# Performance work log

Measured on AMD Instinct MI355X. Metric: run time of the kernel, lower is better.

## Reference

```python
import jax, jax.numpy as jnp
import numpy as np

TEMPERATURE = 8.0  # sqrt(d_k=64)

def setup_inputs() -> dict:
    key = jax.random.key(0)
    kq, kk, kv, km1, km2 = jax.random.split(key, 5)
    B, Lq, Lk, D = 128, 512, 512, 64
    q = jax.random.normal(kq, (B, Lq, D), dtype=jnp.float32)
    k = jax.random.normal(kk, (B, Lk, D), dtype=jnp.float32)
    v = jax.random.normal(kv, (B, Lk, D), dtype=jnp.float32)
    key_mask = jax.random.bernoulli(km1, 0.5, (B, Lq, Lk))
    query_mask = jax.random.bernoulli(km2, 0.5, (B, Lq, Lk))
    return {"q": q, "k": k, "v": v, "key_mask": key_mask, "query_mask": query_mask}

def reference(q, k, v, key_mask, query_mask):
    # attn = (q @ k^T) / temperature, pre-softmax key masking with -inf
    scores = jnp.einsum('bqd,bkd->bqk', q, k) / TEMPERATURE
    scores = jnp.where(key_mask, -jnp.inf, scores)
    attn = jax.nn.softmax(scores, axis=-1)
    # post-softmax query-row zeroing
    attn = jnp.where(query_mask, 0.0, attn)
    # dropout omitted (eval mode / deterministic reference)
    output = jnp.einsum('bqk,bkd->bqd', attn, v)
    return (output, attn)
```

## Files before the change

### kernel.cpp

```cpp
#include <hip/hip_runtime.h>
#include <hip/hip_bf16.h>

#define BATCH 128
#define LQ    512
#define LK    512
#define DH    64
#define TQ    16
#define SSTR  520
#define VROW  72

#define WS_K 0
#define WS_V 4194304
#define WS_Q 8388608
#define WS_BYTES 25165824ull

typedef float    float4v __attribute__((ext_vector_type(4)));
typedef short    short8v __attribute__((ext_vector_type(8)));
typedef short    short4v __attribute__((ext_vector_type(4)));
typedef int      int4v   __attribute__((ext_vector_type(4)));
typedef _Float16 half4v  __attribute__((ext_vector_type(4)));

__device__ __forceinline__ short bf16r(float f) {
  union { float f; unsigned u; } x; x.f = f;
  unsigned r = x.u + 0x7FFFu + ((x.u >> 16) & 1u);
  return (short)(r >> 16);
}

__global__ __launch_bounds__(256)
void prep_kernel(const float* __restrict__ Q, const float* __restrict__ K,
                 const float* __restrict__ V, short* __restrict__ ws)
{
  const int bid = blockIdx.x, tid = threadIdx.x;
  if (bid < 1024) {
    __shared__ short T[64 * VROW];
    const int b  = bid >> 3;
    const int k0 = (bid & 7) * 64;
    const int bR = tid >> 4;
    const int bC = tid & 15;
    const float* vp = V + ((size_t)(b * LK + k0 + bR * 4)) * DH + bC * 4;
    float4v r0 = *(const float4v*)(vp);
    float4v r1 = *(const float4v*)(vp + DH);
    float4v r2 = *(const float4v*)(vp + 2 * DH);
    float4v r3 = *(const float4v*)(vp + 3 * DH);
#pragma unroll
    for (int e = 0; e < 4; ++e) {
      int d  = bC * 4 + e;
      int gp = bR ^ (d & 15);
      short4v s4;
      s4[0] = bf16r(r0[e]); s4[1] = bf16r(r1[e]);
      s4[2] = bf16r(r2[e]); s4[3] = bf16r(r3[e]);
      *(short4v*)&T[d * VROW + gp * 4] = s4;
    }
    __syncthreads();
    const int d  = tid >> 2;
    const int g0 = (tid & 3) * 4;
    short v16[16];
#pragma unroll
    for (int s2 = 0; s2 < 4; ++s2) {
      int g = g0 + s2;
      short4v t4 = *(const short4v*)&T[d * VROW + ((g ^ (d & 15)) * 4)];
      v16[s2 * 4 + 0] = t4[0]; v16[s2 * 4 + 1] = t4[1];
      v16[s2 * 4 + 2] = t4[2]; v16[s2 * 4 + 3] = t4[3];
    }
    short* dst = ws + WS_V + ((size_t)(b * DH + d)) * LK + k0 + g0 * 4;
    *(short8v*)(dst)     = *(short8v*)&v16[0];
    *(short8v*)(dst + 8) = *(short8v*)&v16[8];
  } else {
    const bool isK = (bid < 1152);
    const size_t base = (size_t)((isK ? bid - 1024 : bid - 1152)) * 32768;
    const float* src = (isK ? K : Q) + base;
    short* dst = ws + (isK ? WS_K : WS_Q) + base;
#pragma unroll 4
    for (int u = 0; u < 32; ++u) {
      float4v f = *(const float4v*)(src + u * 1024 + tid * 4);
      short4v s4;
      s4[0] = bf16r(f[0]); s4[1] = bf16r(f[1]);
      s4[2] = bf16r(f[2]); s4[3] = bf16r(f[3]);
      *(short4v*)(dst + u * 1024 + tid * 4) = s4;
    }
  }
}

__global__ __launch_bounds__(256, 4)
void sdpa_main(const short* __restrict__ Kbf, const short* __restrict__ Vt,
               const short* __restrict__ Qbf, const int* __restrict__ KM,
               const int* __restrict__ QM, float* __restrict__ OUT,
               float* __restrict__ ATT)
{
  __shared__ short sc[TQ * SSTR];
  __shared__ float cmb[2][64];

  const int bid  = blockIdx.x;
  const int wg   = ((bid & 7) << 9) | (bid >> 3);
  const int b    = wg >> 5;
  const int q0   = (wg & 31) * TQ;
  const int tid  = threadIdx.x;
  const int lane = tid & 63;
  const int wv   = tid >> 6;
  const int lm   = lane & 15;
  const int quad = lane >> 4;

  const size_t qg    = (size_t)(b * LQ + q0 + lm);
  const size_t mbase = qg * LK + wv * 128 + quad * 4;

  int4v kmv[8];
#pragma unroll
  for (int t = 0; t < 8; ++t)
    kmv[t] = __builtin_nontemporal_load((const int4v*)(KM + mbase + t * 16));

  const short* qp = Qbf + qg * DH + quad * 8;
  const short8v qb0 = *(const short8v*)(qp);
  const short8v qb1 = *(const short8v*)(qp + 32);

  float s[32];
  const short* kp0 = Kbf + ((size_t)(b * LK + wv * 128 + lm)) * DH + quad * 8;
#pragma unroll
  for (int t = 0; t < 8; ++t) {
    const short* kp = kp0 + (size_t)t * 16 * DH;
    short8v ka0 = *(const short8v*)(kp);
    short8v ka1 = *(const short8v*)(kp + 32);
    float4v acc = {0.f, 0.f, 0.f, 0.f};
    acc = __builtin_amdgcn_mfma_f32_16x16x32_bf16(ka0, qb0, acc, 0, 0, 0);
    acc = __builtin_amdgcn_mfma_f32_16x16x32_bf16(ka1, qb1, acc, 0, 0, 0);
#pragma unroll
    for (int j = 0; j < 4; ++j) s[t * 4 + j] = acc[j];
  }

  float mx0 = -INFINITY, mx1 = -INFINITY, mx2 = -INFINITY, mx3 = -INFINITY;
#pragma unroll
  for (int t = 0; t < 8; ++t) {
#pragma unroll
    for (int e = 0; e < 4; ++e) {
      float v = kmv[t][e] ? -INFINITY : s[t * 4 + e];
      s[t * 4 + e] = v;
      if (e == 0) mx0 = fmaxf(mx0, v);
      else if (e == 1) mx1 = fmaxf(mx1, v);
      else if (e == 2) mx2 = fmaxf(mx2, v);
      else mx3 = fmaxf(mx3, v);
    }
  }
  float mx = fmaxf(fmaxf(mx0, mx1), fmaxf(mx2, mx3));
  mx = fmaxf(mx, __shfl_xor(mx, 16, 64));
  mx = fmaxf(mx, __shfl_xor(mx, 32, 64));

  int4v qmv[8];
#pragma unroll
  for (int t = 0; t < 8; ++t)
    qmv[t] = __builtin_nontemporal_load((const int4v*)(QM + mbase + t * 16));

  if (lane < 16) cmb[0][wv * 16 + lane] = mx;
  __syncthreads();
  mx = fmaxf(fmaxf(cmb[0][lm], cmb[0][16 + lm]),
             fmaxf(cmb[0][32 + lm], cmb[0][48 + lm]));

  float s0 = 0.f, s1 = 0.f, s2 = 0.f, s3 = 0.f;
#pragma unroll
  for (int t = 0; t < 8; ++t) {
    float p0 = __expf((s[t * 4 + 0] - mx) * 0.125f);
    float p1 = __expf((s[t * 4 + 1] - mx) * 0.125f);
    float p2 = __expf((s[t * 4 + 2] - mx) * 0.125f);
    float p3 = __expf((s[t * 4 + 3] - mx) * 0.125f);
    s[t * 4 + 0] = p0; s[t * 4 + 1] = p1;
    s[t * 4 + 2] = p2; s[t * 4 + 3] = p3;
    s0 += p0; s1 += p1; s2 += p2; s3 += p3;
  }
  float sum = (s0 + s1) + (s2 + s3);
  sum += __shfl_xor(sum, 16, 64);
  sum += __shfl_xor(sum, 32, 64);
  if (lane < 16) cmb[1][wv * 16 + lane] = sum;
  __syncthreads();
  sum = (cmb[1][lm] + cmb[1][16 + lm]) + (cmb[1][32 + lm] + cmb[1][48 + lm]);
  const float inv = __builtin_amdgcn_rcpf(sum);

  float* arow = ATT + mbase;
  short* srow = &sc[lm * SSTR + wv * 128 + quad * 4];
#pragma unroll
  for (int t = 0; t < 8; ++t) {
    float4v a4;
#pragma unroll
    for (int e = 0; e < 4; ++e)
      a4[e] = qmv[t][e] ? 0.f : s[t * 4 + e] * inv;
    __builtin_nontemporal_store(a4, (float4v*)(arow + t * 16));
    short4v ab;
    ab[0] = bf16r(a4[0]); ab[1] = bf16r(a4[1]);
    ab[2] = bf16r(a4[2]); ab[3] = bf16r(a4[3]);
    *(short4v*)(srow + t * 16) = ab;
  }
  __syncthreads();

  float4v oa = {0.f, 0.f, 0.f, 0.f}, ob = {0.f, 0.f, 0.f, 0.f};
  const short* ap = &sc[lm * SSTR + quad * 8];
  const short* vp = Vt + ((size_t)(b * DH + wv * 16 + lm)) * LK + quad * 8;
#pragma unroll
  for (int c = 0; c < 16; c += 2) {
    short8v a0 = *(const short8v*)(ap + c * 32);
    short8v b0 = *(const short8v*)(vp + c * 32);
    short8v a1 = *(const short8v*)(ap + (c + 1) * 32);
    short8v b1 = *(const short8v*)(vp + (c + 1) * 32);
    oa = __builtin_amdgcn_mfma_f32_16x16x32_bf16(a0, b0, oa, 0, 0, 0);
    ob = __builtin_amdgcn_mfma_f32_16x16x32_bf16(a1, b1, ob, 0, 0, 0);
  }
  float4v oacc = oa + ob;
  float* obase = OUT + ((size_t)(b * LQ + q0 + quad * 4)) * DH + wv * 16 + lm;
  obase[0 * DH] = oacc[0];
  obase[1 * DH] = oacc[1];
  obase[2 * DH] = oacc[2];
  obase[3 * DH] = oacc[3];
}

__global__ __launch_bounds__(256, 4)
void sdpa_fallback(const float* __restrict__ Q, const float* __restrict__ K,
                   const float* __restrict__ V, const int* __restrict__ KM,
                   const int* __restrict__ QM, float* __restrict__ OUT,
                   float* __restrict__ ATT)
{
  __shared__ short kvs[64 * VROW];
  __shared__ short scs[TQ * SSTR];
  const int bid  = blockIdx.x;
  const int wg   = ((bid & 7) << 9) | (bid >> 3);
  const int b    = wg >> 5;
  const int q0   = (wg & 31) * TQ;
  const int tid  = threadIdx.x;
  const int lane = tid & 63;
  const int wave = tid >> 6;
  const int lm   = lane & 15;
  const int quad = lane >> 4;
  const int row  = tid >> 4;
  const int col  = tid & 15;
  const size_t gro = (size_t)(b * LQ + q0 + row) * LK;
  int4v km8[8];
#pragma unroll
  for (int j = 0; j < 8; ++j)
    km8[j] = __builtin_nontemporal_load((const int4v*)(KM + gro + col * 4 + j * 64));
  const float* qrow = Q + ((size_t)(b * LQ + q0 + lm)) * DH + quad * 8;
  short8v aq0, aq1;
  {
    float4v f0 = *(const float4v*)(qrow + 0);
    float4v f1 = *(const float4v*)(qrow + 4);
    float4v f2 = *(const float4v*)(qrow + 32);
    float4v f3 = *(const float4v*)(qrow + 36);
#pragma unroll
    for (int e = 0; e < 4; ++e) {
      aq0[e] = bf16r(f0[e]); aq0[e + 4] = bf16r(f1[e]);
      aq1[e] = bf16r(f2[e]); aq1[e + 4] = bf16r(f3[e]);
    }
  }
  unsigned kb = 0;
#pragma unroll
  for (int j = 0; j < 8; ++j)
#pragma unroll
    for (int e = 0; e < 4; ++e) kb |= (unsigned)(km8[j][e] != 0) << (j * 4 + e);
  const float* kbp = K + ((size_t)(b * LK + lm)) * DH + quad * 8;
#pragma unroll
  for (int t = 0; t < 8; ++t) {
    const float* kr = kbp + (size_t)(wave * 8 + t) * 16 * DH;
    float4v f0 = *(const float4v*)(kr + 0);
    float4v f1 = *(const float4v*)(kr + 4);
    float4v f2 = *(const float4v*)(kr + 32);
    float4v f3 = *(const float4v*)(kr + 36);
    short8v b0, b1;
#pragma unroll
    for (int e = 0; e < 4; ++e) {
      b0[e] = bf16r(f0[e]); b0[e + 4] = bf16r(f1[e]);
      b1[e] = bf16r(f2[e]); b1[e + 4] = bf16r(f3[e]);
    }
    float4v acc = {0.f, 0.f, 0.f, 0.f};
    acc = __builtin_amdgcn_mfma_f32_16x16x32_bf16(aq0, b0, acc, 0, 0, 0);
    acc = __builtin_amdgcn_mfma_f32_16x16x32_bf16(aq1, b1, acc, 0, 0, 0);
    const int n = (wave * 8 + t) * 16 + lm;
#pragma unroll
    for (int j = 0; j < 4; ++j)
      *(_Float16*)&scs[(quad * 4 + j) * SSTR + n] = (_Float16)acc[j];
  }
  int4v qm8[8];
#pragma unroll
  for (int j = 0; j < 8; ++j)
    qm8[j] = __builtin_nontemporal_load((const int4v*)(QM + gro + col * 4 + j * 64));
  __syncthreads();
  float s[32];
  float mx = -INFINITY;
#pragma unroll
  for (int j = 0; j < 8; ++j) {
    half4v h4 = *(const half4v*)&scs[row * SSTR + col * 4 + j * 64];
#pragma unroll
    for (int e = 0; e < 4; ++e) {
      float val = ((kb >> (j * 4 + e)) & 1u) ? -INFINITY : (float)h4[e];
      s[j * 4 + e] = val;
      mx = fmaxf(mx, val);
    }
  }
#pragma unroll
  for (int off = 8; off; off >>= 1) mx = fmaxf(mx, __shfl_xor(mx, off, 64));
  unsigned qb = 0;
#pragma unroll
  for (int j = 0; j < 8; ++j)
#pragma unroll
    for (int e = 0; e < 4; ++e) qb |= (unsigned)(qm8[j][e] != 0) << (j * 4 + e);
  float sum = 0.f;
#pragma unroll
  for (int j = 0; j < 32; ++j) {
    float p = __expf((s[j] - mx) * 0.125f);
    s[j] = p; sum += p;
  }
#pragma unroll
  for (int off = 8; off; off >>= 1) sum += __shfl_xor(sum, off, 64);
  const float inv = 1.f / sum;
  float* arow = ATT + gro;
#pragma unroll
  for (int j = 0; j < 8; ++j) {
    int kk = col * 4 + j * 64;
    float4v a4;
#pragma unroll
    for (int e = 0; e < 4; ++e)
      a4[e] = ((qb >> (j * 4 + e)) & 1u) ? 0.f : s[j * 4 + e] * inv;
    *(float4v*)(arow + kk) = a4;
    short4v ab;
    ab[0] = bf16r(a4[0]); ab[1] = bf16r(a4[1]);
    ab[2] = bf16r(a4[2]); ab[3] = bf16r(a4[3]);
    *(short4v*)&scs[row * SSTR + kk] = ab;
  }
  float4v oacc = {0.f, 0.f, 0.f, 0.f};
  const float* vbase = V + ((size_t)b * LK) * DH;
#pragma unroll
  for (int kt = 0; kt < 8; ++kt) {
    const float* vp = vbase + (kt * 64 + row * 4) * DH + col * 4;
    float4v r0 = *(const float4v*)(vp);
    float4v r1 = *(const float4v*)(vp + DH);
    float4v r2 = *(const float4v*)(vp + 2 * DH);
    float4v r3 = *(const float4v*)(vp + 3 * DH);
#pragma unroll
    for (int e = 0; e < 4; ++e) {
      int d = col * 4 + e;
      int gp = row ^ (d & 15);
      short4v s4;
      s4[0] = bf16r(r0[e]); s4[1] = bf16r(r1[e]);
      s4[2] = bf16r(r2[e]); s4[3] = bf16r(r3[e]);
      *(short4v*)&kvs[d * VROW + gp * 4] = s4;
    }
    __syncthreads();
#pragma unroll
    for (int ks = 0; ks < 2; ++ks) {
      const short* ap = &scs[lm * SSTR + kt * 64 + ks * 32 + quad * 8];
      short8v a8 = *(const short8v*)ap;
      int n  = wave * 16 + lm;
      int g0 = ks * 8 + quad * 2;
      short4v lo = *(const short4v*)&kvs[n * VROW + ((g0) ^ (n & 15)) * 4];
      short4v hi = *(const short4v*)&kvs[n * VROW + ((g0 + 1) ^ (n & 15)) * 4];
      short8v b8;
      b8[0] = lo[0]; b8[1] = lo[1]; b8[2] = lo[2]; b8[3] = lo[3];
      b8[4] = hi[0]; b8[5] = hi[1]; b8[6] = hi[2]; b8[7] = hi[3];
      oacc = __builtin_amdgcn_mfma_f32_16x16x32_bf16(a8, b8, oacc, 0, 0, 0);
    }
    __syncthreads();
  }
  float* obase = OUT + ((size_t)(b * LQ + q0 + quad * 4)) * DH + wave * 16 + lm;
  obase[0 * DH] = oacc[0];
  obase[1 * DH] = oacc[1];
  obase[2 * DH] = oacc[2];
  obase[3 * DH] = oacc[3];
}

extern "C" void kernel_launch(void* const* d_in, const int* in_sizes, int n_in,
                              void* d_out, int out_size, void* d_ws, size_t ws_size,
                              hipStream_t stream) {
  const float* q  = (const float*)d_in[0];
  const float* k  = (const float*)d_in[1];
  const float* v  = (const float*)d_in[2];
  const int*   km = (const int*)d_in[3];
  const int*   qm = (const int*)d_in[4];
  float* out  = (float*)d_out;
  float* attn = out + (size_t)BATCH * LQ * DH;
  if (d_ws != nullptr && ws_size >= WS_BYTES) {
    short* ws = (short*)d_ws;
    hipLaunchKernelGGL(prep_kernel, dim3(1280), dim3(256), 0, stream, q, k, v, ws);
    hipLaunchKernelGGL(sdpa_main, dim3(BATCH * (LQ / TQ)), dim3(256), 0, stream,
                       ws + WS_K, ws + WS_V, ws + WS_Q, km, qm, out, attn);
  } else {
    hipLaunchKernelGGL(sdpa_fallback, dim3(BATCH * (LQ / TQ)), dim3(256), 0, stream,
                       q, k, v, km, qm, out, attn);
  }
}
```

Measured before the change: 422.4 us.

## Pack boolean masks into bitfields in prep kernel before main attention pass

Adds mask-packing blocks to the prep kernel that read both int32 masks and write them as 32-bit bitfields into the workspace. The main kernel then loads one word per lane per mask instead of eight 16-byte vectors each. The aim is to cut register pressure and load latency in the main kernel. In exchange the full mask bytes are still read once, plus an extra write and read of the packed masks. Attention stores also switch from nontemporal to regular, and a raw-mask variant is kept for smaller workspaces.

```diff
diff --git a/kernel.cpp b/kernel.cpp
--- a/kernel.cpp
+++ b/kernel.cpp
@@ -12,7 +12,9 @@
 #define WS_K 0
 #define WS_V 4194304
 #define WS_Q 8388608
-#define WS_BYTES 25165824ull
+#define WS_MB_SHORT 12582912
+#define WS_BYTES_QKV 25165824ull
+#define WS_BYTES_FULL 33554432ull
 
 typedef float    float4v __attribute__((ext_vector_type(4)));
 typedef short    short8v __attribute__((ext_vector_type(8)));
@@ -28,7 +30,8 @@
 
 __global__ __launch_bounds__(256)
 void prep_kernel(const float* __restrict__ Q, const float* __restrict__ K,
-                 const float* __restrict__ V, short* __restrict__ ws)
+                 const float* __restrict__ V, const int* __restrict__ KM,
+                 const int* __restrict__ QM, short* __restrict__ ws)
 {
   const int bid = blockIdx.x, tid = threadIdx.x;
   if (bid < 1024) {
@@ -65,7 +68,7 @@
     short* dst = ws + WS_V + ((size_t)(b * DH + d)) * LK + k0 + g0 * 4;
     *(short8v*)(dst)     = *(short8v*)&v16[0];
     *(short8v*)(dst + 8) = *(short8v*)&v16[8];
-  } else {
+  } else if (bid < 1280) {
     const bool isK = (bid < 1152);
     const size_t base = (size_t)((isK ? bid - 1024 : bid - 1152)) * 32768;
     const float* src = (isK ? K : Q) + base;
@@ -78,14 +81,38 @@
       s4[2] = bf16r(f[2]); s4[3] = bf16r(f[3]);
       *(short4v*)(dst + u * 1024 + tid * 4) = s4;
     }
+  } else {
+    const bool isKM = (bid < 2304);
+    const int  mi   = bid - (isKM ? 1280 : 2304);
+    const int  b    = mi >> 3;
+    const int  q0   = (mi & 7) * 64;
+    const int  ql   = tid >> 2;
+    const int  wv   = tid & 3;
+    const int* src  = (isKM ? KM : QM) +
+                      ((size_t)(b * LQ + q0 + ql)) * LK + wv * 128;
+    unsigned bits[4] = {0u, 0u, 0u, 0u};
+#pragma unroll
+    for (int t = 0; t < 8; ++t) {
+#pragma unroll
+      for (int quad = 0; quad < 4; ++quad) {
+        int4v m4 = *(const int4v*)(src + t * 16 + quad * 4);
+#pragma unroll
+        for (int e = 0; e < 4; ++e)
+          bits[quad] |= (unsigned)(m4[e] != 0) << (t * 4 + e);
+      }
+    }
+    unsigned* mb = (unsigned*)(ws + WS_MB_SHORT) + (isKM ? 0u : 1048576u);
+    *(int4v*)(mb + ((size_t)(b * LQ + q0 + ql)) * 16 + wv * 4) =
+        *(const int4v*)bits;
   }
 }
 
 __global__ __launch_bounds__(256, 4)
-void sdpa_main(const short* __restrict__ Kbf, const short* __restrict__ Vt,
-               const short* __restrict__ Qbf, const int* __restrict__ KM,
-               const int* __restrict__ QM, float* __restrict__ OUT,
-               float* __restrict__ ATT)
+void sdpa_main_packed(const short* __restrict__ Kbf, const short* __restrict__ Vt,
+                      const short* __restrict__ Qbf,
+                      const unsigned* __restrict__ KMB,
+                      const unsigned* __restrict__ QMB,
+                      float* __restrict__ OUT, float* __restrict__ ATT)
 {
   __shared__ short sc[TQ * SSTR];
   __shared__ float cmb[2][64];
@@ -103,10 +130,8 @@
   const size_t qg    = (size_t)(b * LQ + q0 + lm);
   const size_t mbase = qg * LK + wv * 128 + quad * 4;
 
-  int4v kmv[8];
-#pragma unroll
-  for (int t = 0; t < 8; ++t)
-    kmv[t] = __builtin_nontemporal_load((const int4v*)(KM + mbase + t * 16));
+  const unsigned kb  = KMB[qg * 16 + wv * 4 + quad];
+  const unsigned qmb = QMB[qg * 16 + wv * 4 + quad];
 
   const short* qp = Qbf + qg * DH + quad * 8;
   const short8v qb0 = *(const short8v*)(qp);
@@ -131,7 +156,7 @@
   for (int t = 0; t < 8; ++t) {
 #pragma unroll
     for (int e = 0; e < 4; ++e) {
-      float v = kmv[t][e] ? -INFINITY : s[t * 4 + e];
+      float v = ((kb >> (t * 4 + e)) & 1u) ? -INFINITY : s[t * 4 + e];
       s[t * 4 + e] = v;
       if (e == 0) mx0 = fmaxf(mx0, v);
       else if (e == 1) mx1 = fmaxf(mx1, v);
@@ -142,12 +167,6 @@
   float mx = fmaxf(fmaxf(mx0, mx1), fmaxf(mx2, mx3));
   mx = fmaxf(mx, __shfl_xor(mx, 16, 64));
   mx = fmaxf(mx, __shfl_xor(mx, 32, 64));
-
-  int4v qmv[8];
-#pragma unroll
-  for (int t = 0; t < 8; ++t)
-    qmv[t] = __builtin_nontemporal_load((const int4v*)(QM + mbase + t * 16));
-
   if (lane < 16) cmb[0][wv * 16 + lane] = mx;
   __syncthreads();
   mx = fmaxf(fmaxf(cmb[0][lm], cmb[0][16 + lm]),
@@ -179,8 +198,8 @@
     float4v a4;
 #pragma unroll
     for (int e = 0; e < 4; ++e)
-      a4[e] = qmv[t][e] ? 0.f : s[t * 4 + e] * inv;
-    __builtin_nontemporal_store(a4, (float4v*)(arow + t * 16));
+      a4[e] = ((qmb >> (t * 4 + e)) & 1u) ? 0.f : s[t * 4 + e] * inv;
+    *(float4v*)(arow + t * 16) = a4;
     short4v ab;
     ab[0] = bf16r(a4[0]); ab[1] = bf16r(a4[1]);
     ab[2] = bf16r(a4[2]); ab[3] = bf16r(a4[3]);
@@ -188,6 +207,113 @@
   }
   __syncthreads();
 
+  float4v oa = {0.f, 0.f, 0.f, 0.f}, ob = {0.f, 0.f, 0.f, 0.f};
+  const short* ap = &sc[lm * SSTR + quad * 8];
+  const short* vp = Vt + ((size_t)(b * DH + wv * 16 + lm)) * LK + quad * 8;
+#pragma unroll
+  for (int c = 0; c < 16; c += 2) {
+    short8v a0 = *(const short8v*)(ap + c * 32);
+    short8v b0 = *(const short8v*)(vp + c * 32);
+    short8v a1 = *(const short8v*)(ap + (c + 1) * 32);
+    short8v b1 = *(const short8v*)(vp + (c + 1) * 32);
+    oa = __builtin_amdgcn_mfma_f32_16x16x32_bf16(a0, b0, oa, 0, 0, 0);
+    ob = __builtin_amdgcn_mfma_f32_16x16x32_bf16(a1, b1, ob, 0, 0, 0);
+  }
+  float4v oacc = oa + ob;
+  float* obase = OUT + ((size_t)(b * LQ + q0 + quad * 4)) * DH + wv * 16 + lm;
+  obase[0 * DH] = oacc[0];
+  obase[1 * DH] = oacc[1];
+  obase[2 * DH] = oacc[2];
+  obase[3 * DH] = oacc[3];
+}
+
+__global__ __launch_bounds__(256, 4)
+void sdpa_main_raw(const short* __restrict__ Kbf, const short* __restrict__ Vt,
+                   const short* __restrict__ Qbf, const int* __restrict__ KM,
+                   const int* __restrict__ QM, float* __restrict__ OUT,
+                   float* __restrict__ ATT)
+{
+  __shared__ short sc[TQ * SSTR];
+  __shared__ float cmb[2][64];
+  const int bid  = blockIdx.x;
+  const int wg   = ((bid & 7) << 9) | (bid >> 3);
+  const int b    = wg >> 5;
+  const int q0   = (wg & 31) * TQ;
+  const int tid  = threadIdx.x;
+  const int lane = tid & 63;
+  const int wv   = tid >> 6;
+  const int lm   = lane & 15;
+  const int quad = lane >> 4;
+  const size_t qg    = (size_t)(b * LQ + q0 + lm);
+  const size_t mbase = qg * LK + wv * 128 + quad * 4;
+  int4v kmv[8];
+#pragma unroll
+  for (int t = 0; t < 8; ++t)
+    kmv[t] = __builtin_nontemporal_load((const int4v*)(KM + mbase + t * 16));
+  const short* qp = Qbf + qg * DH + quad * 8;
+  const short8v qb0 = *(const short8v*)(qp);
+  const short8v qb1 = *(const short8v*)(qp + 32);
+  float s[32];
+  const short* kp0 = Kbf + ((size_t)(b * LK + wv * 128 + lm)) * DH + quad * 8;
+#pragma unroll
+  for (int t = 0; t < 8; ++t) {
+    const short* kp = kp0 + (size_t)t * 16 * DH;
+    short8v ka0 = *(const short8v*)(kp);
+    short8v ka1 = *(const short8v*)(kp + 32);
+    float4v acc = {0.f, 0.f, 0.f, 0.f};
+    acc = __builtin_amdgcn_mfma_f32_16x16x32_bf16(ka0, qb0, acc, 0, 0, 0);
+    acc = __builtin_amdgcn_mfma_f32_16x16x32_bf16(ka1, qb1, acc, 0, 0, 0);
+#pragma unroll
+    for (int j = 0; j < 4; ++j) s[t * 4 + j] = acc[j];
+  }
+  float mx = -INFINITY;
+#pragma unroll
+  for (int t = 0; t < 8; ++t)
+#pragma unroll
+    for (int e = 0; e < 4; ++e) {
+      float v = kmv[t][e] ? -INFINITY : s[t * 4 + e];
+      s[t * 4 + e] = v;
+      mx = fmaxf(mx, v);
+    }
+  mx = fmaxf(mx, __shfl_xor(mx, 16, 64));
+  mx = fmaxf(mx, __shfl_xor(mx, 32, 64));
+  int4v qmv[8];
+#pragma unroll
+  for (int t = 0; t < 8; ++t)
+    qmv[t] = __builtin_nontemporal_load((const int4v*)(QM + mbase + t * 16));
+  if (lane < 16) cmb[0][wv * 16 + lane] = mx;
+  __syncthreads();
+  mx = fmaxf(fmaxf(cmb[0][lm], cmb[0][16 + lm]),
+             fmaxf(cmb[0][32 + lm], cmb[0][48 + lm]));
+  float sum = 0.f;
+#pragma unroll
+  for (int t = 0; t < 8; ++t)
+#pragma unroll
+    for (int e = 0; e < 4; ++e) {
+      float p = __expf((s[t * 4 + e] - mx) * 0.125f);
+      s[t * 4 + e] = p; sum += p;
+    }
+  sum += __shfl_xor(sum, 16, 64);
+  sum += __shfl_xor(sum, 32, 64);
+  if (lane < 16) cmb[1][wv * 16 + lane] = sum;
+  __syncthreads();
+  sum = (cmb[1][lm] + cmb[1][16 + lm]) + (cmb[1][32 + lm] + cmb[1][48 + lm]);
+  const float inv = __builtin_amdgcn_rcpf(sum);
+  float* arow = ATT + mbase;
+  short* srow = &sc[lm * SSTR + wv * 128 + quad * 4];
+#pragma unroll
+  for (int t = 0; t < 8; ++t) {
+    float4v a4;
+#pragma unroll
+    for (int e = 0; e < 4; ++e)
+      a4[e] = qmv[t][e] ? 0.f : s[t * 4 + e] * inv;
+    *(float4v*)(arow + t * 16) = a4;
+    short4v ab;
+    ab[0] = bf16r(a4[0]); ab[1] = bf16r(a4[1]);
+    ab[2] = bf16r(a4[2]); ab[3] = bf16r(a4[3]);
+    *(short4v*)(srow + t * 16) = ab;
+  }
+  __syncthreads();
   float4v oa = {0.f, 0.f, 0.f, 0.f}, ob = {0.f, 0.f, 0.f, 0.f};
   const short* ap = &sc[lm * SSTR + quad * 8];
   const short* vp = Vt + ((size_t)(b * DH + wv * 16 + lm)) * LK + quad * 8;
@@ -231,7 +357,7 @@
   int4v km8[8];
 #pragma unroll
   for (int j = 0; j < 8; ++j)
-    km8[j] = __builtin_nontemporal_load((const int4v*)(KM + gro + col * 4 + j * 64));
+    km8[j] = *(const int4v*)(KM + gro + col * 4 + j * 64);
   const float* qrow = Q + ((size_t)(b * LQ + q0 + lm)) * DH + quad * 8;
   short8v aq0, aq1;
   {
@@ -245,11 +371,11 @@
       aq1[e] = bf16r(f2[e]); aq1[e + 4] = bf16r(f3[e]);
     }
   }
-  unsigned kb = 0;
+  unsigned kbm = 0;
 #pragma unroll
   for (int j = 0; j < 8; ++j)
 #pragma unroll
-    for (int e = 0; e < 4; ++e) kb |= (unsigned)(km8[j][e] != 0) << (j * 4 + e);
+    for (int e = 0; e < 4; ++e) kbm |= (unsigned)(km8[j][e] != 0) << (j * 4 + e);
   const float* kbp = K + ((size_t)(b * LK + lm)) * DH + quad * 8;
 #pragma unroll
   for (int t = 0; t < 8; ++t) {
@@ -275,7 +401,7 @@
   int4v qm8[8];
 #pragma unroll
   for (int j = 0; j < 8; ++j)
-    qm8[j] = __builtin_nontemporal_load((const int4v*)(QM + gro + col * 4 + j * 64));
+    qm8[j] = *(const int4v*)(QM + gro + col * 4 + j * 64);
   __syncthreads();
   float s[32];
   float mx = -INFINITY;
@@ -284,18 +410,18 @@
     half4v h4 = *(const half4v*)&scs[row * SSTR + col * 4 + j * 64];
 #pragma unroll
     for (int e = 0; e < 4; ++e) {
-      float val = ((kb >> (j * 4 + e)) & 1u) ? -INFINITY : (float)h4[e];
+      float val = ((kbm >> (j * 4 + e)) & 1u) ? -INFINITY : (float)h4[e];
       s[j * 4 + e] = val;
       mx = fmaxf(mx, val);
     }
   }
 #pragma unroll
   for (int off = 8; off; off >>= 1) mx = fmaxf(mx, __shfl_xor(mx, off, 64));
-  unsigned qb = 0;
+  unsigned qbm = 0;
 #pragma unroll
   for (int j = 0; j < 8; ++j)
 #pragma unroll
-    for (int e = 0; e < 4; ++e) qb |= (unsigned)(qm8[j][e] != 0) << (j * 4 + e);
+    for (int e = 0; e < 4; ++e) qbm |= (unsigned)(qm8[j][e] != 0) << (j * 4 + e);
   float sum = 0.f;
 #pragma unroll
   for (int j = 0; j < 32; ++j) {
@@ -312,7 +438,7 @@
     float4v a4;
 #pragma unroll
     for (int e = 0; e < 4; ++e)
-      a4[e] = ((qb >> (j * 4 + e)) & 1u) ? 0.f : s[j * 4 + e] * inv;
+      a4[e] = ((qbm >> (j * 4 + e)) & 1u) ? 0.f : s[j * 4 + e] * inv;
     *(float4v*)(arow + kk) = a4;
     short4v ab;
     ab[0] = bf16r(a4[0]); ab[1] = bf16r(a4[1]);
@@ -370,13 +496,24 @@
   const int*   qm = (const int*)d_in[4];
   float* out  = (float*)d_out;
   float* attn = out + (size_t)BATCH * LQ * DH;
-  if (d_ws != nullptr && ws_size >= WS_BYTES) {
+  if (d_ws != nullptr && ws_size >= WS_BYTES_FULL) {
     short* ws = (short*)d_ws;
-    hipLaunchKernelGGL(prep_kernel, dim3(1280), dim3(256), 0, stream, q, k, v, ws);
-    hipLaunchKernelGGL(sdpa_main, dim3(BATCH * (LQ / TQ)), dim3(256), 0, stream,
-                       ws + WS_K, ws + WS_V, ws + WS_Q, km, qm, out, attn);
+    const unsigned* kmb = (const unsigned*)(ws + WS_MB_SHORT);
+    const unsigned* qmb = kmb + 1048576;
+    hipLaunchKernelGGL(prep_kernel, dim3(3328), dim3(256), 0, stream,
+                       q, k, v, km, qm, ws);
+    hipLaunchKernelGGL(sdpa_main_packed, dim3(BATCH * (LQ / TQ)), dim3(256), 0,
+                       stream, ws + WS_K, ws + WS_V, ws + WS_Q, kmb, qmb,
+                       out, attn);
+  } else if (d_ws != nullptr && ws_size >= WS_BYTES_QKV) {
+    short* ws = (short*)d_ws;
+    hipLaunchKernelGGL(prep_kernel, dim3(1280), dim3(256), 0, stream,
+                       q, k, v, km, qm, ws);
+    hipLaunchKernelGGL(sdpa_main_raw, dim3(BATCH * (LQ / TQ)), dim3(256), 0,
+                       stream, ws + WS_K, ws + WS_V, ws + WS_Q, km, qm,
+                       out, attn);
   } else {
-    hipLaunchKernelGGL(sdpa_fallback, dim3(BATCH * (LQ / TQ)), dim3(256), 0, stream,
-                       q, k, v, km, qm, out, attn);
+    hipLaunchKernelGGL(sdpa_fallback, dim3(BATCH * (LQ / TQ)), dim3(256), 0,
+                       stream, q, k, v, km, qm, out, attn);
   }
 }
```

Measured after the change: 447.4 us. 5.9% more time.

## Pack mask rows into bitmasks via wave ballots and shared memory

Applied to the files above, without the earlier changes.

The main kernel now reads both mask rows with coalesced per-lane loads, packs them into 32-bit bitmasks with wave ballots, and hands them to each thread through a small shared-memory table. This replaces the per-thread int4 mask vectors that were held in registers. The goal is to cut register pressure, which allows raising the launch-bounds occupancy hint from 4 to 6. Other changes: the input loads in the prep kernel become nontemporal, the attention-matrix stores go from nontemporal to regular, and the fallback kernel's mask loads lose their nontemporal hint. The extra barrier and ballot work add latency before the softmax.

```diff
diff --git a/kernel.cpp b/kernel.cpp
--- a/kernel.cpp
+++ b/kernel.cpp
@@ -12,7 +12,7 @@
 #define WS_K 0
 #define WS_V 4194304
 #define WS_Q 8388608
-#define WS_BYTES 25165824ull
+#define WS_BYTES_QKV 25165824ull
 
 typedef float    float4v __attribute__((ext_vector_type(4)));
 typedef short    short8v __attribute__((ext_vector_type(8)));
@@ -38,10 +38,10 @@
     const int bR = tid >> 4;
     const int bC = tid & 15;
     const float* vp = V + ((size_t)(b * LK + k0 + bR * 4)) * DH + bC * 4;
-    float4v r0 = *(const float4v*)(vp);
-    float4v r1 = *(const float4v*)(vp + DH);
-    float4v r2 = *(const float4v*)(vp + 2 * DH);
-    float4v r3 = *(const float4v*)(vp + 3 * DH);
+    float4v r0 = __builtin_nontemporal_load((const float4v*)(vp));
+    float4v r1 = __builtin_nontemporal_load((const float4v*)(vp + DH));
+    float4v r2 = __builtin_nontemporal_load((const float4v*)(vp + 2 * DH));
+    float4v r3 = __builtin_nontemporal_load((const float4v*)(vp + 3 * DH));
 #pragma unroll
     for (int e = 0; e < 4; ++e) {
       int d  = bC * 4 + e;
@@ -72,7 +72,7 @@
     short* dst = ws + (isK ? WS_K : WS_Q) + base;
 #pragma unroll 4
     for (int u = 0; u < 32; ++u) {
-      float4v f = *(const float4v*)(src + u * 1024 + tid * 4);
+      float4v f = __builtin_nontemporal_load((const float4v*)(src + u * 1024 + tid * 4));
       short4v s4;
       s4[0] = bf16r(f[0]); s4[1] = bf16r(f[1]);
       s4[2] = bf16r(f[2]); s4[3] = bf16r(f[3]);
@@ -81,14 +81,15 @@
   }
 }
 
-__global__ __launch_bounds__(256, 4)
-void sdpa_main(const short* __restrict__ Kbf, const short* __restrict__ Vt,
-               const short* __restrict__ Qbf, const int* __restrict__ KM,
-               const int* __restrict__ QM, float* __restrict__ OUT,
-               float* __restrict__ ATT)
+__global__ __launch_bounds__(256, 6)
+void sdpa_fused(const short* __restrict__ Kbf, const short* __restrict__ Vt,
+                const short* __restrict__ Qbf, const int* __restrict__ KM,
+                const int* __restrict__ QM,
+                float* __restrict__ OUT, float* __restrict__ ATT)
 {
   __shared__ short sc[TQ * SSTR];
   __shared__ float cmb[2][64];
+  __shared__ unsigned pk[2][16][17];
 
   const int bid  = blockIdx.x;
   const int wg   = ((bid & 7) << 9) | (bid >> 3);
@@ -100,13 +101,32 @@
   const int lm   = lane & 15;
   const int quad = lane >> 4;
 
+#pragma unroll
+  for (int m = 0; m < 2; ++m) {
+    const int* srcb = m ? QM : KM;
+#pragma unroll
+    for (int r = 0; r < 4; ++r) {
+      const int rr = wv * 4 + r;
+      const int* src = srcb + ((size_t)(b * LQ + q0 + rr)) * LK;
+      unsigned long long B[8];
+#pragma unroll
+      for (int j = 0; j < 8; ++j) {
+        int mv = __builtin_nontemporal_load(src + j * 64 + lane);
+        B[j] = __ballot(mv != 0);
+      }
+      if (lane < 16) {
+        const int wvv = lane >> 2, qd = lane & 3;
+        unsigned long long blo = (B[2 * wvv]     >> (qd * 4)) & 0x000F000F000F000FULL;
+        unsigned long long bhi = (B[2 * wvv + 1] >> (qd * 4)) & 0x000F000F000F000FULL;
+        unsigned lo = (unsigned)((blo | (blo >> 12) | (blo >> 24) | (blo >> 36)) & 0xFFFFull);
+        unsigned hi = (unsigned)((bhi | (bhi >> 12) | (bhi >> 24) | (bhi >> 36)) & 0xFFFFull);
+        pk[m][rr][lane] = lo | (hi << 16);
+      }
+    }
+  }
+
   const size_t qg    = (size_t)(b * LQ + q0 + lm);
   const size_t mbase = qg * LK + wv * 128 + quad * 4;
-
-  int4v kmv[8];
-#pragma unroll
-  for (int t = 0; t < 8; ++t)
-    kmv[t] = __builtin_nontemporal_load((const int4v*)(KM + mbase + t * 16));
 
   const short* qp = Qbf + qg * DH + quad * 8;
   const short8v qb0 = *(const short8v*)(qp);
@@ -126,12 +146,16 @@
     for (int j = 0; j < 4; ++j) s[t * 4 + j] = acc[j];
   }
 
+  __syncthreads();
+  const unsigned kb  = pk[0][lm][wv * 4 + quad];
+  const unsigned qmb = pk[1][lm][wv * 4 + quad];
+
   float mx0 = -INFINITY, mx1 = -INFINITY, mx2 = -INFINITY, mx3 = -INFINITY;
 #pragma unroll
   for (int t = 0; t < 8; ++t) {
 #pragma unroll
     for (int e = 0; e < 4; ++e) {
-      float v = kmv[t][e] ? -INFINITY : s[t * 4 + e];
+      float v = ((kb >> (t * 4 + e)) & 1u) ? -INFINITY : s[t * 4 + e];
       s[t * 4 + e] = v;
       if (e == 0) mx0 = fmaxf(mx0, v);
       else if (e == 1) mx1 = fmaxf(mx1, v);
@@ -142,12 +166,6 @@
   float mx = fmaxf(fmaxf(mx0, mx1), fmaxf(mx2, mx3));
   mx = fmaxf(mx, __shfl_xor(mx, 16, 64));
   mx = fmaxf(mx, __shfl_xor(mx, 32, 64));
-
-  int4v qmv[8];
-#pragma unroll
-  for (int t = 0; t < 8; ++t)
-    qmv[t] = __builtin_nontemporal_load((const int4v*)(QM + mbase + t * 16));
-
   if (lane < 16) cmb[0][wv * 16 + lane] = mx;
   __syncthreads();
   mx = fmaxf(fmaxf(cmb[0][lm], cmb[0][16 + lm]),
@@ -179,8 +197,8 @@
     float4v a4;
 #pragma unroll
     for (int e = 0; e < 4; ++e)
-      a4[e] = qmv[t][e] ? 0.f : s[t * 4 + e] * inv;
-    __builtin_nontemporal_store(a4, (float4v*)(arow + t * 16));
+      a4[e] = ((qmb >> (t * 4 + e)) & 1u) ? 0.f : s[t * 4 + e] * inv;
+    *(float4v*)(arow + t * 16) = a4;
     short4v ab;
     ab[0] = bf16r(a4[0]); ab[1] = bf16r(a4[1]);
     ab[2] = bf16r(a4[2]); ab[3] = bf16r(a4[3]);
@@ -231,7 +249,7 @@
   int4v km8[8];
 #pragma unroll
   for (int j = 0; j < 8; ++j)
-    km8[j] = __builtin_nontemporal_load((const int4v*)(KM + gro + col * 4 + j * 64));
+    km8[j] = *(const int4v*)(KM + gro + col * 4 + j * 64);
   const float* qrow = Q + ((size_t)(b * LQ + q0 + lm)) * DH + quad * 8;
   short8v aq0, aq1;
   {
@@ -245,11 +263,11 @@
       aq1[e] = bf16r(f2[e]); aq1[e + 4] = bf16r(f3[e]);
     }
   }
-  unsigned kb = 0;
+  unsigned kbm = 0;
 #pragma unroll
   for (int j = 0; j < 8; ++j)
 #pragma unroll
-    for (int e = 0; e < 4; ++e) kb |= (unsigned)(km8[j][e] != 0) << (j * 4 + e);
+    for (int e = 0; e < 4; ++e) kbm |= (unsigned)(km8[j][e] != 0) << (j * 4 + e);
   const float* kbp = K + ((size_t)(b * LK + lm)) * DH + quad * 8;
 #pragma unroll
   for (int t = 0; t < 8; ++t) {
@@ -275,7 +293,7 @@
   int4v qm8[8];
 #pragma unroll
   for (int j = 0; j < 8; ++j)
-    qm8[j] = __builtin_nontemporal_load((const int4v*)(QM + gro + col * 4 + j * 64));
+    qm8[j] = *(const int4v*)(QM + gro + col * 4 + j * 64);
   __syncthreads();
   float s[32];
   float mx = -INFINITY;
@@ -284,18 +302,18 @@
     half4v h4 = *(const half4v*)&scs[row * SSTR + col * 4 + j * 64];
 #pragma unroll
     for (int e = 0; e < 4; ++e) {
-      float val = ((kb >> (j * 4 + e)) & 1u) ? -INFINITY : (float)h4[e];
+      float val = ((kbm >> (j * 4 + e)) & 1u) ? -INFINITY : (float)h4[e];
       s[j * 4 + e] = val;
       mx = fmaxf(mx, val);
     }
   }
 #pragma unroll
   for (int off = 8; off; off >>= 1) mx = fmaxf(mx, __shfl_xor(mx, off, 64));
-  unsigned qb = 0;
+  unsigned qbm = 0;
 #pragma unroll
   for (int j = 0; j < 8; ++j)
 #pragma unroll
-    for (int e = 0; e < 4; ++e) qb |= (unsigned)(qm8[j][e] != 0) << (j * 4 + e);
+    for (int e = 0; e < 4; ++e) qbm |= (unsigned)(qm8[j][e] != 0) << (j * 4 + e);
   float sum = 0.f;
 #pragma unroll
   for (int j = 0; j < 32; ++j) {
@@ -312,7 +330,7 @@
     float4v a4;
 #pragma unroll
     for (int e = 0; e < 4; ++e)
-      a4[e] = ((qb >> (j * 4 + e)) & 1u) ? 0.f : s[j * 4 + e] * inv;
+      a4[e] = ((qbm >> (j * 4 + e)) & 1u) ? 0.f : s[j * 4 + e] * inv;
     *(float4v*)(arow + kk) = a4;
     short4v ab;
     ab[0] = bf16r(a4[0]); ab[1] = bf16r(a4[1]);
@@ -370,13 +388,15 @@
   const int*   qm = (const int*)d_in[4];
   float* out  = (float*)d_out;
   float* attn = out + (size_t)BATCH * LQ * DH;
-  if (d_ws != nullptr && ws_size >= WS_BYTES) {
+  if (d_ws != nullptr && ws_size >= WS_BYTES_QKV) {
     short* ws = (short*)d_ws;
-    hipLaunchKernelGGL(prep_kernel, dim3(1280), dim3(256), 0, stream, q, k, v, ws);
-    hipLaunchKernelGGL(sdpa_main, dim3(BATCH * (LQ / TQ)), dim3(256), 0, stream,
-                       ws + WS_K, ws + WS_V, ws + WS_Q, km, qm, out, attn);
+    hipLaunchKernelGGL(prep_kernel, dim3(1280), dim3(256), 0, stream,
+                       q, k, v, ws);
+    hipLaunchKernelGGL(sdpa_fused, dim3(BATCH * (LQ / TQ)), dim3(256), 0,
+                       stream, ws + WS_K, ws + WS_V, ws + WS_Q, km, qm,
+                       out, attn);
   } else {
-    hipLaunchKernelGGL(sdpa_fallback, dim3(BATCH * (LQ / TQ)), dim3(256), 0, stream,
-                       q, k, v, km, qm, out, attn);
+    hipLaunchKernelGGL(sdpa_fallback, dim3(BATCH * (LQ / TQ)), dim3(256), 0,
+                       stream, q, k, v, km, qm, out, attn);
   }
 }
```

Result: faster. 403.4 us (-4.5%).
